# Performance work log

Measured on AMD Instinct MI355X. Metric: run time of the kernel, lower is better.

The kernel has to match this reference:

```python
import jax, jax.numpy as jnp
import numpy as np

VOCAB, EMBED, HIDDEN = 32000, 512, 1024
BATCH, SEQ = 32, 48
PAD = 0


def setup_inputs() -> dict:
    key = jax.random.key(0)
    ks = jax.random.split(key, 10)
    s = 0.02
    emb = jax.random.normal(ks[0], (VOCAB, EMBED), jnp.float32) * s
    emb = emb.at[PAD].set(0.0)  # padding_idx row zeroed
    return {
        "inputs": jax.random.randint(ks[1], (BATCH, SEQ), 0, VOCAB),
        "hidden": jax.random.normal(ks[2], (BATCH, HIDDEN), jnp.float32),
        "cell": jax.random.normal(ks[3], (BATCH, HIDDEN), jnp.float32),
        "emb": emb,
        "W_ih": jax.random.normal(ks[4], (4 * HIDDEN, EMBED), jnp.float32) * s,
        "W_hh": jax.random.normal(ks[5], (4 * HIDDEN, HIDDEN), jnp.float32) * s,
        "b_ih": jnp.zeros((4 * HIDDEN,), jnp.float32),
        "b_hh": jnp.zeros((4 * HIDDEN,), jnp.float32),
        "fc_W": jax.random.normal(ks[6], (VOCAB, HIDDEN), jnp.float32) * s,
        "fc_b": jnp.zeros((VOCAB,), jnp.float32),
        "generate_len": 50,
    }


def reference(inputs, hidden, cell, emb, W_ih, W_hh, b_ih, b_hh, fc_W, fc_b, generate_len):
    # Training-path forward (dropout treated as identity for determinism).
    x = emb[inputs]                      # [B, S, E]
    xs = jnp.transpose(x, (1, 0, 2))     # [S, B, E] time-major

    def step(carry, x_t):
        h, c = carry
        gates = x_t @ W_ih.T + b_ih + h @ W_hh.T + b_hh  # [B, 4H]
        i, f, g, o = jnp.split(gates, 4, axis=-1)
        c_new = jax.nn.sigmoid(f) * c + jax.nn.sigmoid(i) * jnp.tanh(g)
        h_new = jax.nn.sigmoid(o) * jnp.tanh(c_new)
        logits = h_new @ fc_W.T + fc_b                   # [B, V]
        return (h_new, c_new), logits

    _, out = jax.lax.scan(step, (hidden, cell), xs)      # [S, B, V]
    return jnp.transpose(out, (1, 0, 2))                 # [B, S, V]
```

## Files before the change

### kernel.cpp

```cpp
#include <hip/hip_runtime.h>
#include <stdint.h>


typedef unsigned short u16;
typedef __attribute__((ext_vector_type(8))) short bf16x8;
typedef __attribute__((ext_vector_type(4))) float floatx4;
struct alignas(8) us4 { u16 x, y, z, w; };

#define BATCH 32
#define SEQ   48
#define EMBED 512
#define HID   1024
#define VOCAB 32000
#define MROWS (SEQ * BATCH)

__device__ __forceinline__ u16 f2bf(float f) {
  unsigned u = __float_as_uint(f);
  u += 0x7FFF + ((u >> 16) & 1);
  return (u16)(u >> 16);
}

__device__ __forceinline__ floatx4 mfma16(bf16x8 a, bf16x8 b, floatx4 c) {
  return __builtin_amdgcn_mfma_f32_16x16x32_bf16(a, b, c, 0, 0, 0);
}

typedef __attribute__((address_space(1))) unsigned int as1_uint;
typedef __attribute__((address_space(3))) unsigned int as3_uint;
__device__ __forceinline__ void gl_lds16(const void* g, void* l) {
  __builtin_amdgcn_global_load_lds((as1_uint*)g, (as3_uint*)l, 16, 0, 0);
}

__device__ __forceinline__ float sigmoidf_(float x) {
  return 1.0f / (1.0f + __expf(-x));
}

__device__ __forceinline__ void ld_c16(bf16x8& d, const u16* p) {
  asm volatile("global_load_dwordx4 %0, %1, off sc0 sc1" : "=&v"(d) : "v"(p));
}
__device__ __forceinline__ void ld_n16(bf16x8& d, const u16* p) {
  asm volatile("global_load_dwordx4 %0, %1, off" : "=&v"(d) : "v"(p));
}

#define BAR_U32S 576

__global__ void cast_kernel(const float* __restrict__ in, u16* __restrict__ out, int n4) {
  int i = blockIdx.x * blockDim.x + threadIdx.x;
  if (i < n4) {
    float4 v = *(const float4*)(in + (size_t)i * 4);
    us4 o;
    o.x = f2bf(v.x); o.y = f2bf(v.y); o.z = f2bf(v.z); o.w = f2bf(v.w);
    *(us4*)(out + (size_t)i * 4) = o;
  }
}

__global__ void gather_kernel(const int* __restrict__ idx, const float* __restrict__ emb,
                              u16* __restrict__ X, unsigned* __restrict__ bar) {
  int bid = blockIdx.x;
  if (bid == 0) {
    for (int j = threadIdx.x; j < BAR_U32S; j += 128) bar[j] = 0u;
  }
  int s = bid >> 5, b = bid & 31;
  int t = idx[b * SEQ + s];
  const float* src = emb + (size_t)t * EMBED;
  u16* dst = X + (size_t)bid * EMBED;
  int e = threadIdx.x * 4;
  float4 v = *(const float4*)(src + e);
  us4 o;
  o.x = f2bf(v.x); o.y = f2bf(v.y); o.z = f2bf(v.z); o.w = f2bf(v.w);
  *(us4*)(dst + e) = o;
}

__global__ __launch_bounds__(256) void gemm_bt_kernel(
    const u16* __restrict__ A, const u16* __restrict__ B,
    const float* __restrict__ bias0, const float* __restrict__ bias1,
    float* __restrict__ C, int M, int N, int K, int out_mode) {
  __shared__ u16 As[128 * 64];
  __shared__ u16 Bs[128 * 64];

  const int tid = threadIdx.x;
  const int wave = tid >> 6, lane = tid & 63;
  const int l3 = lane >> 3, l7 = lane & 7;
  const int q = lane >> 4, rf = lane & 15;
  const int tn = blockIdx.x, tm = blockIdx.y;
  const int gm0 = tm * 128, gn0 = tn * 128;
  const int wm = (wave & 1) * 64, wn = (wave >> 1) * 64;

  floatx4 acc[4][4];
#pragma unroll
  for (int i = 0; i < 4; ++i)
#pragma unroll
    for (int j = 0; j < 4; ++j) acc[i][j] = (floatx4){0.f, 0.f, 0.f, 0.f};

  for (int k0 = 0; k0 < K; k0 += 64) {
#pragma unroll
    for (int i = 0; i < 4; ++i) {
      int e = wave * 4 + i;
      int r = e * 8 + l3;
      int qd = l7 ^ (r & 7);
      gl_lds16(A + (size_t)(gm0 + r) * K + k0 + qd * 8, (void*)(As + e * 512));
      gl_lds16(B + (size_t)(gn0 + r) * K + k0 + qd * 8, (void*)(Bs + e * 512));
    }
    __syncthreads();

#pragma unroll
    for (int kk = 0; kk < 64; kk += 32) {
      int jc = (kk >> 3) + q;
      bf16x8 af[4], bf[4];
#pragma unroll
      for (int mi = 0; mi < 4; ++mi) {
        int r = wm + mi * 16 + rf;
        af[mi] = *(const bf16x8*)(As + r * 64 + (jc ^ (r & 7)) * 8);
      }
#pragma unroll
      for (int ni = 0; ni < 4; ++ni) {
        int r = wn + ni * 16 + rf;
        bf[ni] = *(const bf16x8*)(Bs + r * 64 + (jc ^ (r & 7)) * 8);
      }
#pragma unroll
      for (int mi = 0; mi < 4; ++mi)
#pragma unroll
        for (int ni = 0; ni < 4; ++ni)
          acc[mi][ni] = mfma16(af[mi], bf[ni], acc[mi][ni]);
    }
    __syncthreads();
  }

#pragma unroll
  for (int ni = 0; ni < 4; ++ni) {
    int n = gn0 + wn + ni * 16 + rf;
    float bv = bias0[n];
    if (bias1) bv += bias1[n];
#pragma unroll
    for (int mi = 0; mi < 4; ++mi) {
#pragma unroll
      for (int r = 0; r < 4; ++r) {
        int m = gm0 + wm + mi * 16 + q * 4 + r;
        float val = acc[mi][ni][r] + bv;
        if (out_mode == 0) {
          C[(size_t)m * N + n] = val;
        } else {
          int b = m & 31, s = m >> 5;
          C[((size_t)b * SEQ + s) * N + n] = val;
        }
      }
    }
  }
}

__global__ __launch_bounds__(256, 1) void lstm_persist3_kernel(
    const u16* __restrict__ Whh,
    const float* __restrict__ xg_all,
    const float* __restrict__ c_init,
    u16* __restrict__ Hall,
    unsigned* __restrict__ bar) {
  const int bid = blockIdx.x;
  const int u0 = bid * 4;
  const int tid = threadIdx.x;
  const int wave = tid >> 6, lane = tid & 63;
  const int q = lane >> 4, rf = lane & 15;
  const int gate = rf >> 2, du = rf & 3;
  const int brow = gate * HID + u0 + du;

  __shared__ float red[4][32][16];

  const int ab = tid >> 2, ad = tid & 3;
  float c_reg = 0.f;
  if (tid < 128) c_reg = c_init[ab * HID + u0 + ad];

  const u16* wp = Whh + (size_t)brow * HID + wave * 256 + q * 8;
  unsigned* gcnt   = bar + (bid & 7) * 64;
  unsigned* root    = bar + 512;
  unsigned* release = bar + 544;

  for (int s = 0; s < SEQ; ++s) {
    const u16* h_prev = Hall + (size_t)s * BATCH * HID;
    const float* xg = xg_all + (size_t)s * BATCH * 4096;
    const u16* a0p = h_prev + (size_t)rf * HID + wave * 256 + q * 8;
    const u16* a1p = a0p + 16 * HID;

    float xgv[4];
    if (tid < 128) {
#pragma unroll
      for (int gt = 0; gt < 4; ++gt) xgv[gt] = xg[ab * 4096 + gt * HID + u0 + ad];
    }

    bf16x8 wv[8], a0v[8], a1v[8];
#pragma unroll
    for (int i = 0; i < 8; ++i) {
      ld_n16(wv[i], wp + i * 32);
      ld_c16(a0v[i], a0p + i * 32);
      ld_c16(a1v[i], a1p + i * 32);
    }
    asm volatile("s_waitcnt vmcnt(0)" ::: "memory");
    __builtin_amdgcn_sched_barrier(0);

    floatx4 acc0 = {0.f, 0.f, 0.f, 0.f}, acc1 = {0.f, 0.f, 0.f, 0.f};
#pragma unroll
    for (int i = 0; i < 8; ++i) {
      acc0 = mfma16(a0v[i], wv[i], acc0);
      acc1 = mfma16(a1v[i], wv[i], acc1);
    }

#pragma unroll
    for (int r = 0; r < 4; ++r) {
      red[wave][q * 4 + r][rf] = acc0[r];
      red[wave][16 + q * 4 + r][rf] = acc1[r];
    }
    __syncthreads();

    if (tid < 128) {
      float g4[4];
#pragma unroll
      for (int gt = 0; gt < 4; ++gt) {
        int n = gt * 4 + ad;
        float v = red[0][ab][n] + red[1][ab][n] + red[2][ab][n] + red[3][ab][n];
        g4[gt] = v + xgv[gt];
      }
      float i_ = sigmoidf_(g4[0]);
      float f_ = sigmoidf_(g4[1]);
      float gg = tanhf(g4[2]);
      float o_ = sigmoidf_(g4[3]);
      c_reg = f_ * c_reg + i_ * gg;
      float hv = o_ * tanhf(c_reg);
      u16 hb = f2bf(hv);
      float hn = __shfl_xor(hv, 1);
      u16 nb = f2bf(hn);
      if ((tid & 1) == 0) {
        unsigned w = (unsigned)hb | ((unsigned)nb << 16);
        unsigned* dst = (unsigned*)(Hall + (size_t)(s + 1) * BATCH * HID +
                                    ab * HID + u0 + ad);
        __hip_atomic_store(dst, w, __ATOMIC_RELAXED, __HIP_MEMORY_SCOPE_AGENT);
      }
    }
    __syncthreads();
    if (tid == 0) {
      unsigned old = __hip_atomic_fetch_add(gcnt, 1u, __ATOMIC_RELAXED,
                                            __HIP_MEMORY_SCOPE_AGENT);
      if (old + 1 == 32u * (unsigned)(s + 1)) {
        unsigned r = __hip_atomic_fetch_add(root, 1u, __ATOMIC_RELAXED,
                                            __HIP_MEMORY_SCOPE_AGENT);
        if (r + 1 == 8u * (unsigned)(s + 1)) {
          __hip_atomic_store(release, (unsigned)(s + 1), __ATOMIC_RELAXED,
                             __HIP_MEMORY_SCOPE_AGENT);
        }
      }
      while (__hip_atomic_load(release, __ATOMIC_RELAXED,
                               __HIP_MEMORY_SCOPE_AGENT) < (unsigned)(s + 1))
        __builtin_amdgcn_s_sleep(2);
    }
    __syncthreads();
  }
}

extern "C" void kernel_launch(void* const* d_in, const int* in_sizes, int n_in,
                              void* d_out, int out_size, void* d_ws, size_t ws_size,
                              hipStream_t stream) {
  const int*   inputs = (const int*)d_in[0];
  const float* hidden = (const float*)d_in[1];
  const float* cell   = (const float*)d_in[2];
  const float* emb    = (const float*)d_in[3];
  const float* W_ih   = (const float*)d_in[4];
  const float* W_hh   = (const float*)d_in[5];
  const float* b_ih   = (const float*)d_in[6];
  const float* b_hh   = (const float*)d_in[7];
  const float* fc_W   = (const float*)d_in[8];
  const float* fc_b   = (const float*)d_in[9];
  float* out = (float*)d_out;

  char* ws = (char*)d_ws;
  u16*   Xbf  = (u16*)(ws);
  u16*   Wihb = (u16*)(ws + 1572864);
  u16*   Whhb = (u16*)(ws + 1572864 + 4194304);
  u16*   fcWb = (u16*)(ws + 14155776);
  float* Xg   = (float*)(ws + 14155776 + 65536000);
  u16*   Hall = (u16*)(ws + 104857600);
  unsigned* bar = (unsigned*)(ws + 104857600 + 3211264);

  cast_kernel<<<(4096 * 512 / 4 + 255) / 256, 256, 0, stream>>>(W_ih, Wihb, 4096 * 512 / 4);
  cast_kernel<<<(4096 * 1024 / 4 + 255) / 256, 256, 0, stream>>>(W_hh, Whhb, 4096 * 1024 / 4);
  cast_kernel<<<(VOCAB * 1024 / 4 + 255) / 256, 256, 0, stream>>>(fc_W, fcWb, VOCAB * 1024 / 4);
  cast_kernel<<<(BATCH * HID / 4 + 255) / 256, 256, 0, stream>>>(hidden, Hall, BATCH * HID / 4);

  gather_kernel<<<MROWS, 128, 0, stream>>>(inputs, emb, Xbf, bar);

  gemm_bt_kernel<<<dim3(4096 / 128, MROWS / 128), 256, 0, stream>>>(
      Xbf, Wihb, b_ih, b_hh, Xg, MROWS, 4096, EMBED, 0);

  lstm_persist3_kernel<<<256, 256, 0, stream>>>(Whhb, Xg, cell, Hall, bar);

  gemm_bt_kernel<<<dim3(VOCAB / 128, MROWS / 128), 256, 0, stream>>>(
      Hall + (size_t)BATCH * HID, fcWb, fc_b, (const float*)nullptr, out,
      MROWS, VOCAB, HID, 1);
}
```

Baseline: 801.2 us.

## Merge cast kernels, keep W_hh in registers, split barrier, widen output GEMM tile

Four weight/hidden cast launches become one combined kernel. The persistent LSTM kernel now loads its W_hh slice into registers once instead of every step. The grid barrier is split into arrive and wait, with the next step's input-gate prefetch between them, and the trailing barrier after the last step is dropped. The vocab projection GEMM uses a new 256x128 tile with 512 threads, which halves B-tile reloads, at the cost of more LDS and fewer blocks.

```diff
diff --git a/kernel.cpp b/kernel.cpp
--- a/kernel.cpp
+++ b/kernel.cpp
@@ -43,14 +43,21 @@
 
 #define BAR_U32S 576
 
-__global__ void cast_kernel(const float* __restrict__ in, u16* __restrict__ out, int n4) {
+__global__ void cast_all_kernel(const float* __restrict__ s0, u16* __restrict__ d0, int n0,
+                                const float* __restrict__ s1, u16* __restrict__ d1, int n1,
+                                const float* __restrict__ s2, u16* __restrict__ d2, int n2,
+                                const float* __restrict__ s3, u16* __restrict__ d3, int n3) {
   int i = blockIdx.x * blockDim.x + threadIdx.x;
-  if (i < n4) {
-    float4 v = *(const float4*)(in + (size_t)i * 4);
-    us4 o;
-    o.x = f2bf(v.x); o.y = f2bf(v.y); o.z = f2bf(v.z); o.w = f2bf(v.w);
-    *(us4*)(out + (size_t)i * 4) = o;
-  }
+  const float* src; u16* dst; int off;
+  if (i < n0)                     { src = s0; dst = d0; off = i; }
+  else if (i < n0 + n1)           { src = s1; dst = d1; off = i - n0; }
+  else if (i < n0 + n1 + n2)      { src = s2; dst = d2; off = i - n0 - n1; }
+  else if (i < n0 + n1 + n2 + n3) { src = s3; dst = d3; off = i - n0 - n1 - n2; }
+  else return;
+  float4 v = *(const float4*)(src + (size_t)off * 4);
+  us4 o;
+  o.x = f2bf(v.x); o.y = f2bf(v.y); o.z = f2bf(v.z); o.w = f2bf(v.w);
+  *(us4*)(dst + (size_t)off * 4) = o;
 }
 
 __global__ void gather_kernel(const int* __restrict__ idx, const float* __restrict__ emb,
@@ -73,7 +80,7 @@
 __global__ __launch_bounds__(256) void gemm_bt_kernel(
     const u16* __restrict__ A, const u16* __restrict__ B,
     const float* __restrict__ bias0, const float* __restrict__ bias1,
-    float* __restrict__ C, int M, int N, int K, int out_mode) {
+    float* __restrict__ C, int M, int N, int K) {
   __shared__ u16 As[128 * 64];
   __shared__ u16 Bs[128 * 64];
 
@@ -135,19 +142,90 @@
 #pragma unroll
       for (int r = 0; r < 4; ++r) {
         int m = gm0 + wm + mi * 16 + q * 4 + r;
-        float val = acc[mi][ni][r] + bv;
-        if (out_mode == 0) {
-          C[(size_t)m * N + n] = val;
-        } else {
-          int b = m & 31, s = m >> 5;
-          C[((size_t)b * SEQ + s) * N + n] = val;
-        }
-      }
-    }
-  }
-}
-
-__global__ __launch_bounds__(256, 1) void lstm_persist3_kernel(
+        C[(size_t)m * N + n] = acc[mi][ni][r] + bv;
+      }
+    }
+  }
+}
+
+__global__ __launch_bounds__(512) void gemm_bt256_kernel(
+    const u16* __restrict__ A, const u16* __restrict__ B,
+    const float* __restrict__ bias0, float* __restrict__ C,
+    int N, int K) {
+  __shared__ u16 As[256 * 64];
+  __shared__ u16 Bs[128 * 64];
+
+  const int tid = threadIdx.x;
+  const int wave = tid >> 6, lane = tid & 63;
+  const int l3 = lane >> 3, l7 = lane & 7;
+  const int q = lane >> 4, rf = lane & 15;
+  const int tn = blockIdx.x, tm = blockIdx.y;
+  const int gm0 = tm * 256, gn0 = tn * 128;
+  const int wm = (wave & 3) * 64, wn = (wave >> 2) * 64;
+
+  floatx4 acc[4][4];
+#pragma unroll
+  for (int i = 0; i < 4; ++i)
+#pragma unroll
+    for (int j = 0; j < 4; ++j) acc[i][j] = (floatx4){0.f, 0.f, 0.f, 0.f};
+
+  for (int k0 = 0; k0 < K; k0 += 64) {
+#pragma unroll
+    for (int i = 0; i < 6; ++i) {
+      int e = wave * 6 + i;
+      if (e < 32) {
+        int r = e * 8 + l3;
+        int qd = l7 ^ (r & 7);
+        gl_lds16(A + (size_t)(gm0 + r) * K + k0 + qd * 8, (void*)(As + e * 512));
+      } else {
+        int e2 = e - 32;
+        int r = e2 * 8 + l3;
+        int qd = l7 ^ (r & 7);
+        gl_lds16(B + (size_t)(gn0 + r) * K + k0 + qd * 8, (void*)(Bs + e2 * 512));
+      }
+    }
+    __syncthreads();
+
+#pragma unroll
+    for (int kk = 0; kk < 64; kk += 32) {
+      int jc = (kk >> 3) + q;
+      bf16x8 af[4], bf[4];
+#pragma unroll
+      for (int mi = 0; mi < 4; ++mi) {
+        int r = wm + mi * 16 + rf;
+        af[mi] = *(const bf16x8*)(As + r * 64 + (jc ^ (r & 7)) * 8);
+      }
+#pragma unroll
+      for (int ni = 0; ni < 4; ++ni) {
+        int r = wn + ni * 16 + rf;
+        bf[ni] = *(const bf16x8*)(Bs + r * 64 + (jc ^ (r & 7)) * 8);
+      }
+#pragma unroll
+      for (int mi = 0; mi < 4; ++mi)
+#pragma unroll
+        for (int ni = 0; ni < 4; ++ni)
+          acc[mi][ni] = mfma16(af[mi], bf[ni], acc[mi][ni]);
+    }
+    __syncthreads();
+  }
+
+#pragma unroll
+  for (int ni = 0; ni < 4; ++ni) {
+    int n = gn0 + wn + ni * 16 + rf;
+    float bv = bias0[n];
+#pragma unroll
+    for (int mi = 0; mi < 4; ++mi) {
+#pragma unroll
+      for (int r = 0; r < 4; ++r) {
+        int m = gm0 + wm + mi * 16 + q * 4 + r;
+        int b = m & 31, s = m >> 5;
+        C[((size_t)b * SEQ + s) * N + n] = acc[mi][ni][r] + bv;
+      }
+    }
+  }
+}
+
+__global__ __launch_bounds__(256, 1) void lstm_persist4_kernel(
     const u16* __restrict__ Whh,
     const float* __restrict__ xg_all,
     const float* __restrict__ c_init,
@@ -168,26 +246,35 @@
   if (tid < 128) c_reg = c_init[ab * HID + u0 + ad];
 
   const u16* wp = Whh + (size_t)brow * HID + wave * 256 + q * 8;
-  unsigned* gcnt   = bar + (bid & 7) * 64;
+  bf16x8 wv[8];
+#pragma unroll
+  for (int i = 0; i < 8; ++i) ld_n16(wv[i], wp + i * 32);
+
+  float xgv[4];
+  if (tid < 128) {
+#pragma unroll
+    for (int gt = 0; gt < 4; ++gt) xgv[gt] = xg_all[ab * 4096 + gt * HID + u0 + ad];
+  }
+
+  unsigned* gcnt    = bar + (bid & 7) * 64;
   unsigned* root    = bar + 512;
   unsigned* release = bar + 544;
 
   for (int s = 0; s < SEQ; ++s) {
-    const u16* h_prev = Hall + (size_t)s * BATCH * HID;
-    const float* xg = xg_all + (size_t)s * BATCH * 4096;
-    const u16* a0p = h_prev + (size_t)rf * HID + wave * 256 + q * 8;
+    if (s > 0) {
+      if (tid == 0) {
+        while (__hip_atomic_load(release, __ATOMIC_RELAXED,
+                                 __HIP_MEMORY_SCOPE_AGENT) < (unsigned)s)
+          __builtin_amdgcn_s_sleep(2);
+      }
+      __syncthreads();
+    }
+
+    const u16* a0p = Hall + (size_t)s * BATCH * HID + (size_t)rf * HID + wave * 256 + q * 8;
     const u16* a1p = a0p + 16 * HID;
-
-    float xgv[4];
-    if (tid < 128) {
-#pragma unroll
-      for (int gt = 0; gt < 4; ++gt) xgv[gt] = xg[ab * 4096 + gt * HID + u0 + ad];
-    }
-
-    bf16x8 wv[8], a0v[8], a1v[8];
+    bf16x8 a0v[8], a1v[8];
 #pragma unroll
     for (int i = 0; i < 8; ++i) {
-      ld_n16(wv[i], wp + i * 32);
       ld_c16(a0v[i], a0p + i * 32);
       ld_c16(a1v[i], a1p + i * 32);
     }
@@ -233,22 +320,26 @@
       }
     }
     __syncthreads();
-    if (tid == 0) {
-      unsigned old = __hip_atomic_fetch_add(gcnt, 1u, __ATOMIC_RELAXED,
-                                            __HIP_MEMORY_SCOPE_AGENT);
-      if (old + 1 == 32u * (unsigned)(s + 1)) {
-        unsigned r = __hip_atomic_fetch_add(root, 1u, __ATOMIC_RELAXED,
-                                            __HIP_MEMORY_SCOPE_AGENT);
-        if (r + 1 == 8u * (unsigned)(s + 1)) {
-          __hip_atomic_store(release, (unsigned)(s + 1), __ATOMIC_RELAXED,
-                             __HIP_MEMORY_SCOPE_AGENT);
+
+    if (s < SEQ - 1) {
+      if (tid == 0) {
+        unsigned old = __hip_atomic_fetch_add(gcnt, 1u, __ATOMIC_RELAXED,
+                                              __HIP_MEMORY_SCOPE_AGENT);
+        if (old + 1 == 32u * (unsigned)(s + 1)) {
+          unsigned r = __hip_atomic_fetch_add(root, 1u, __ATOMIC_RELAXED,
+                                              __HIP_MEMORY_SCOPE_AGENT);
+          if (r + 1 == 8u * (unsigned)(s + 1)) {
+            __hip_atomic_store(release, (unsigned)(s + 1), __ATOMIC_RELAXED,
+                               __HIP_MEMORY_SCOPE_AGENT);
+          }
         }
       }
-      while (__hip_atomic_load(release, __ATOMIC_RELAXED,
-                               __HIP_MEMORY_SCOPE_AGENT) < (unsigned)(s + 1))
-        __builtin_amdgcn_s_sleep(2);
-    }
-    __syncthreads();
+      if (tid < 128) {
+        const float* xgn = xg_all + (size_t)(s + 1) * BATCH * 4096;
+#pragma unroll
+        for (int gt = 0; gt < 4; ++gt) xgv[gt] = xgn[ab * 4096 + gt * HID + u0 + ad];
+      }
+    }
   }
 }
 
@@ -276,19 +367,19 @@
   u16*   Hall = (u16*)(ws + 104857600);
   unsigned* bar = (unsigned*)(ws + 104857600 + 3211264);
 
-  cast_kernel<<<(4096 * 512 / 4 + 255) / 256, 256, 0, stream>>>(W_ih, Wihb, 4096 * 512 / 4);
-  cast_kernel<<<(4096 * 1024 / 4 + 255) / 256, 256, 0, stream>>>(W_hh, Whhb, 4096 * 1024 / 4);
-  cast_kernel<<<(VOCAB * 1024 / 4 + 255) / 256, 256, 0, stream>>>(fc_W, fcWb, VOCAB * 1024 / 4);
-  cast_kernel<<<(BATCH * HID / 4 + 255) / 256, 256, 0, stream>>>(hidden, Hall, BATCH * HID / 4);
+  const int n0 = 4096 * 512 / 4, n1 = 4096 * 1024 / 4,
+            n2 = VOCAB * 1024 / 4, n3 = BATCH * HID / 4;
+  const int ncast = n0 + n1 + n2 + n3;
+  cast_all_kernel<<<(ncast + 255) / 256, 256, 0, stream>>>(
+      W_ih, Wihb, n0, W_hh, Whhb, n1, fc_W, fcWb, n2, hidden, Hall, n3);
 
   gather_kernel<<<MROWS, 128, 0, stream>>>(inputs, emb, Xbf, bar);
 
   gemm_bt_kernel<<<dim3(4096 / 128, MROWS / 128), 256, 0, stream>>>(
-      Xbf, Wihb, b_ih, b_hh, Xg, MROWS, 4096, EMBED, 0);
-
-  lstm_persist3_kernel<<<256, 256, 0, stream>>>(Whhb, Xg, cell, Hall, bar);
-
-  gemm_bt_kernel<<<dim3(VOCAB / 128, MROWS / 128), 256, 0, stream>>>(
-      Hall + (size_t)BATCH * HID, fcWb, fc_b, (const float*)nullptr, out,
-      MROWS, VOCAB, HID, 1);
-}
+      Xbf, Wihb, b_ih, b_hh, Xg, MROWS, 4096, EMBED);
+
+  lstm_persist4_kernel<<<256, 256, 0, stream>>>(Whhb, Xg, cell, Hall, bar);
+
+  gemm_bt256_kernel<<<dim3(VOCAB / 128, MROWS / 256), 512, 0, stream>>>(
+      Hall + (size_t)BATCH * HID, fcWb, fc_b, out, VOCAB, HID);
+}
```

Result: faster. 723.8 us (-9.7%).
